# Optimization experiments

Measured on AMD Instinct MI355X. Metric: run time of the kernel, lower is better.

## Reference

```python
import jax, jax.numpy as jnp
import numpy as np

B, S, H, P2 = 64, 512, 768, 46  # batch, seq, hidden, num_p*2


def setup_inputs() -> dict:
    key = jax.random.key(0)
    k1, k2, k3, k4 = jax.random.split(key, 4)
    hidden_states = jax.random.normal(k1, (B, S, H), dtype=jnp.float32)
    # subject start/end indices must lie within the valid (masked-in) prefix
    lengths = jax.random.randint(k2, (B,), S // 4, S + 1)  # cue lengths per sample
    input_mask = (jnp.arange(S)[None, :] < lengths[:, None]).astype(jnp.int32)
    ids = jax.random.randint(k3, (B, 2), 0, S // 4)
    batch_subject_ids = jnp.sort(ids, axis=1).astype(jnp.int32)
    W = jax.random.normal(k4, (P2, H), dtype=jnp.float32) * (1.0 / np.sqrt(H))
    b = jnp.zeros((P2,), dtype=jnp.float32)
    return {"hidden_states": hidden_states, "batch_subject_ids": batch_subject_ids,
            "input_mask": input_mask, "W": W, "b": b}


def reference(hidden_states, batch_subject_ids, input_mask, W, b):
    # per-sample subject embedding: h[b, start] + h[b, end]  -> [B, H]
    batch_idx = jnp.arange(hidden_states.shape[0])
    s = (hidden_states[batch_idx, batch_subject_ids[:, 0]]
         + hidden_states[batch_idx, batch_subject_ids[:, 1]])
    # broadcast-add s to the first cue_len positions of each sample
    cue_len = jnp.sum(input_mask, axis=1)  # [B]
    pos_mask = (jnp.arange(hidden_states.shape[1])[None, :] < cue_len[:, None])  # [B, S]
    h = hidden_states + s[:, None, :] * pos_mask[:, :, None].astype(hidden_states.dtype)
    # linear + sigmoid^4 (dropout is identity in eval mode)
    logits = jnp.einsum('bsh,ph->bsp', h, W) + b
    return jax.nn.sigmoid(logits) ** 4
```

## Files before the change

kernel.cpp:

```cpp
#include <hip/hip_runtime.h>

#define SEQ 512
#define HID 768
#define P2  46
#define BLK 512
#define MT  128
#define KC  32
#define NC  (HID / KC)
#define WST 776

typedef short bf16x8 __attribute__((ext_vector_type(8)));
typedef float f32x4  __attribute__((ext_vector_type(4)));

__device__ __forceinline__ unsigned short f2bf(float f) {
  union { float f; unsigned int u; } v; v.f = f;
  return (unsigned short)((v.u + 0x7FFFu + ((v.u >> 16) & 1u)) >> 16);
}

__device__ __forceinline__ void gl_lds16(const float* g, void* l) {
  __builtin_amdgcn_global_load_lds(
      (const __attribute__((address_space(1))) void*)g,
      (__attribute__((address_space(3))) void*)l, 16, 0, 0);
}

__global__ __launch_bounds__(BLK, 2) void fused_kernel(const float* __restrict__ h,
                                                       const int* __restrict__ ids,
                                                       const int* __restrict__ mask,
                                                       const float* __restrict__ W,
                                                       const float* __restrict__ bias,
                                                       float* __restrict__ out) {
  __shared__ __align__(16) unsigned short wlds[48 * WST];
  __shared__ __align__(16) float hbuf[4][MT * KC];
  __shared__ __align__(16) float s_lds[HID];
  __shared__ float q_lds[48];

  const int tid  = threadIdx.x;
  const int lane = tid & 63, wv = tid >> 6;
  const int mr   = lane & 15, qd = lane >> 4;
  const int row0 = blockIdx.x * MT;
  const int b    = row0 >> 9;

  auto issueChunk = [&](int c) {
    int buf = c & 3;
    #pragma unroll
    for (int j = 0; j < 2; ++j) {
      int sb  = (wv << 7) + (j << 6);
      int s   = sb + lane;
      int row = s >> 3;
      int cc  = (s & 7) ^ (row & 7);
      const float* g = h + (size_t)(row0 + row) * HID + c * KC + (cc << 2);
      gl_lds16(g, (void*)&hbuf[buf][sb << 2]);
    }
  };

  issueChunk(0); issueChunk(1); issueChunk(2);

  for (int i = tid; i < (2 * WST) / 2; i += BLK)
    ((unsigned int*)(wlds + 46 * WST))[i] = 0u;
  for (int i = tid; i < (P2 * HID) / 4; i += BLK) {
    int r  = i / 192;
    int c0 = (i - r * 192) * 4;
    float4 w4 = *(const float4*)(W + (size_t)r * HID + c0);
    ushort4 v;
    v.x = f2bf(w4.x); v.y = f2bf(w4.y); v.z = f2bf(w4.z); v.w = f2bf(w4.w);
    *(ushort4*)&wlds[r * WST + c0] = v;
  }
  {
    int i0 = ids[b * 2 + 0], i1 = ids[b * 2 + 1];
    const float* r0 = h + ((size_t)b * SEQ + i0) * HID;
    const float* r1 = h + ((size_t)b * SEQ + i1) * HID;
    for (int k = tid; k < HID; k += BLK) s_lds[k] = r0[k] + r1[k];
  }
  __syncthreads();

  if (tid < P2 * 4) {
    int p = tid >> 2, kq = tid & 3;
    const float4* wp = (const float4*)(W + (size_t)p * HID + kq * 192);
    float acc = 0.f;
    #pragma unroll 8
    for (int j = 0; j < 48; ++j) {
      float4 w4 = wp[j];
      int k = kq * 192 + j * 4;
      acc += s_lds[k] * w4.x + s_lds[k + 1] * w4.y
           + s_lds[k + 2] * w4.z + s_lds[k + 3] * w4.w;
    }
    acc += __shfl_xor(acc, 1, 64);
    acc += __shfl_xor(acc, 2, 64);
    if (kq == 0) q_lds[p] = acc;
  }
  __syncthreads();

  f32x4 acc[3];
  #pragma unroll
  for (int nt = 0; nt < 3; ++nt) acc[nt] = f32x4{0.f, 0.f, 0.f, 0.f};

  const int rA   = (wv << 4) + mr;
  const int base = (rA & 15) * 8 + (wv << 7);
  const int r7   = mr & 7;

  #pragma unroll
  for (int c = 0; c < NC; ++c) {
    const int fut = NC - 1 - c;
    if (fut >= 2)      asm volatile("s_waitcnt vmcnt(4)" ::: "memory");
    else if (fut == 1) asm volatile("s_waitcnt vmcnt(2)" ::: "memory");
    else               asm volatile("s_waitcnt vmcnt(0)" ::: "memory");

    const float* hb = &hbuf[c & 3][0];
    int cc0 = qd << 1;
    float4 x0 = *(const float4*)&hb[(base + (cc0 ^ r7)) << 2];
    float4 x1 = *(const float4*)&hb[(base + ((cc0 + 1) ^ r7)) << 2];
    bf16x8 a;
    a[0] = (short)f2bf(x0.x); a[1] = (short)f2bf(x0.y);
    a[2] = (short)f2bf(x0.z); a[3] = (short)f2bf(x0.w);
    a[4] = (short)f2bf(x1.x); a[5] = (short)f2bf(x1.y);
    a[6] = (short)f2bf(x1.z); a[7] = (short)f2bf(x1.w);
    #pragma unroll
    for (int nt = 0; nt < 3; ++nt) {
      bf16x8 bb = *(const bf16x8*)&wlds[((nt << 4) + mr) * WST + c * KC + (qd << 3)];
      acc[nt] = __builtin_amdgcn_mfma_f32_16x16x32_bf16(a, bb, acc[nt], 0, 0, 0);
    }
    if (c + 3 < NC) issueChunk(c + 3);
  }

  int mrow[4];
  #pragma unroll
  for (int i = 0; i < 4; ++i)
    mrow[i] = mask[row0 + (wv << 4) + (qd << 2) + i];

  #pragma unroll
  for (int nt = 0; nt < 3; ++nt) {
    int p = (nt << 4) + mr;
    if (p < P2) {
      float bv = bias[p];
      float qv = q_lds[p];
      #pragma unroll
      for (int i = 0; i < 4; ++i) {
        int row = row0 + (wv << 4) + (qd << 2) + i;
        float x = acc[nt][i] + bv + (mrow[i] ? qv : 0.f);
        float sg = 1.f / (1.f + __expf(-x));
        sg *= sg; sg *= sg;
        out[(size_t)row * P2 + p] = sg;
      }
    }
  }
}

extern "C" void kernel_launch(void* const* d_in, const int* in_sizes, int n_in,
                              void* d_out, int out_size, void* d_ws, size_t ws_size,
                              hipStream_t stream) {
  const float* h    = (const float*)d_in[0];
  const int*   ids  = (const int*)d_in[1];
  const int*   mask = (const int*)d_in[2];
  const float* W    = (const float*)d_in[3];
  const float* bias = (const float*)d_in[4];
  float* out = (float*)d_out;

  fused_kernel<<<dim3((64 * SEQ) / MT), BLK, 0, stream>>>(h, ids, mask, W, bias, out);
}
```

Baseline: 169.5 us.

## Split K dimension across two wave groups with LDS reduction in 1024-thread blocks

Doubles the block to 16 waves and splits the hidden dimension in half, so each group of 8 waves computes a partial 128x48 MFMA tile over 12 K-chunks with double buffering. Partial accumulators are then combined through LDS before the sigmoid epilogue. The subject-projection dot product is redistributed so each wave reduces whole rows with shuffles. The goal is more waves in flight to hide global-load latency, at the cost of an extra LDS reduction, shallower prefetch and larger blocks per CU.

Result: faster. 163.4 us (-3.6%).

```diff
diff --git a/kernel.cpp b/kernel.cpp
--- a/kernel.cpp
+++ b/kernel.cpp
@@ -3,10 +3,10 @@
 #define SEQ 512
 #define HID 768
 #define P2  46
-#define BLK 512
+#define BLK 1024
 #define MT  128
 #define KC  32
-#define NC  (HID / KC)
+#define HK  12
 #define WST 776
 
 typedef short bf16x8 __attribute__((ext_vector_type(8)));
@@ -23,92 +23,88 @@
       (__attribute__((address_space(3))) void*)l, 16, 0, 0);
 }
 
-__global__ __launch_bounds__(BLK, 2) void fused_kernel(const float* __restrict__ h,
+__global__ __launch_bounds__(BLK, 4) void fused_kernel(const float* __restrict__ h,
                                                        const int* __restrict__ ids,
                                                        const int* __restrict__ mask,
                                                        const float* __restrict__ W,
                                                        const float* __restrict__ bias,
                                                        float* __restrict__ out) {
   __shared__ __align__(16) unsigned short wlds[48 * WST];
-  __shared__ __align__(16) float hbuf[4][MT * KC];
+  __shared__ __align__(16) float hbuf[2][16 * 128 * 4];
   __shared__ __align__(16) float s_lds[HID];
   __shared__ float q_lds[48];
 
   const int tid  = threadIdx.x;
   const int lane = tid & 63, wv = tid >> 6;
+  const int g    = wv & 7,  kh = wv >> 3;
   const int mr   = lane & 15, qd = lane >> 4;
   const int row0 = blockIdx.x * MT;
   const int b    = row0 >> 9;
+  const int c0   = kh * HK;
 
   auto issueChunk = [&](int c) {
-    int buf = c & 3;
+    int buf = c & 1;
     #pragma unroll
     for (int j = 0; j < 2; ++j) {
-      int sb  = (wv << 7) + (j << 6);
-      int s   = sb + lane;
-      int row = s >> 3;
-      int cc  = (s & 7) ^ (row & 7);
-      const float* g = h + (size_t)(row0 + row) * HID + c * KC + (cc << 2);
-      gl_lds16(g, (void*)&hbuf[buf][sb << 2]);
+      int sw = (j << 6) + lane;
+      int rl = sw >> 3;
+      int cc = (sw & 7) ^ (rl & 7);
+      const float* gp = h + (size_t)(row0 + (g << 4) + rl) * HID + c * KC + (cc << 2);
+      gl_lds16(gp, (void*)&hbuf[buf][((wv << 7) + (j << 6)) << 2]);
     }
   };
 
-  issueChunk(0); issueChunk(1); issueChunk(2);
+  issueChunk(c0); issueChunk(c0 + 1);
 
-  for (int i = tid; i < (2 * WST) / 2; i += BLK)
+  for (int i = tid; i < WST; i += BLK)
     ((unsigned int*)(wlds + 46 * WST))[i] = 0u;
   for (int i = tid; i < (P2 * HID) / 4; i += BLK) {
     int r  = i / 192;
-    int c0 = (i - r * 192) * 4;
-    float4 w4 = *(const float4*)(W + (size_t)r * HID + c0);
+    int cb = (i - r * 192) << 2;
+    float4 w4 = *(const float4*)(W + (size_t)r * HID + cb);
     ushort4 v;
     v.x = f2bf(w4.x); v.y = f2bf(w4.y); v.z = f2bf(w4.z); v.w = f2bf(w4.w);
-    *(ushort4*)&wlds[r * WST + c0] = v;
+    *(ushort4*)&wlds[r * WST + cb] = v;
   }
   {
     int i0 = ids[b * 2 + 0], i1 = ids[b * 2 + 1];
     const float* r0 = h + ((size_t)b * SEQ + i0) * HID;
     const float* r1 = h + ((size_t)b * SEQ + i1) * HID;
-    for (int k = tid; k < HID; k += BLK) s_lds[k] = r0[k] + r1[k];
+    if (tid < HID) s_lds[tid] = r0[tid] + r1[tid];
   }
   __syncthreads();
 
-  if (tid < P2 * 4) {
-    int p = tid >> 2, kq = tid & 3;
-    const float4* wp = (const float4*)(W + (size_t)p * HID + kq * 192);
-    float acc = 0.f;
-    #pragma unroll 8
-    for (int j = 0; j < 48; ++j) {
-      float4 w4 = wp[j];
-      int k = kq * 192 + j * 4;
-      acc += s_lds[k] * w4.x + s_lds[k + 1] * w4.y
-           + s_lds[k + 2] * w4.z + s_lds[k + 3] * w4.w;
+  #pragma unroll
+  for (int t = 0; t < 3; ++t) {
+    int p = wv * 3 + t;
+    if (p < P2) {
+      const float* wp = W + (size_t)p * HID;
+      float acc = 0.f;
+      #pragma unroll
+      for (int j = 0; j < HID / 64; ++j)
+        acc += s_lds[(j << 6) + lane] * wp[(j << 6) + lane];
+      #pragma unroll
+      for (int off = 32; off; off >>= 1)
+        acc += __shfl_down(acc, off, 64);
+      if (lane == 0) q_lds[p] = acc;
     }
-    acc += __shfl_xor(acc, 1, 64);
-    acc += __shfl_xor(acc, 2, 64);
-    if (kq == 0) q_lds[p] = acc;
   }
-  __syncthreads();
 
   f32x4 acc[3];
   #pragma unroll
   for (int nt = 0; nt < 3; ++nt) acc[nt] = f32x4{0.f, 0.f, 0.f, 0.f};
 
-  const int rA   = (wv << 4) + mr;
-  const int base = (rA & 15) * 8 + (wv << 7);
-  const int r7   = mr & 7;
+  const int r7    = mr & 7;
+  const int abase = (wv << 7) + (mr << 3);
 
   #pragma unroll
-  for (int c = 0; c < NC; ++c) {
-    const int fut = NC - 1 - c;
-    if (fut >= 2)      asm volatile("s_waitcnt vmcnt(4)" ::: "memory");
-    else if (fut == 1) asm volatile("s_waitcnt vmcnt(2)" ::: "memory");
-    else               asm volatile("s_waitcnt vmcnt(0)" ::: "memory");
-
-    const float* hb = &hbuf[c & 3][0];
-    int cc0 = qd << 1;
-    float4 x0 = *(const float4*)&hb[(base + (cc0 ^ r7)) << 2];
-    float4 x1 = *(const float4*)&hb[(base + ((cc0 + 1) ^ r7)) << 2];
+  for (int i = 0; i < HK; ++i) {
+    int c = c0 + i;
+    if (i < HK - 1) asm volatile("s_waitcnt vmcnt(2)" ::: "memory");
+    else            asm volatile("s_waitcnt vmcnt(0)" ::: "memory");
+    const float* hb = hbuf[c & 1];
+    float4 x0 = *(const float4*)&hb[(abase + (((qd << 1) + 0) ^ r7)) << 2];
+    float4 x1 = *(const float4*)&hb[(abase + (((qd << 1) + 1) ^ r7)) << 2];
     bf16x8 a;
     a[0] = (short)f2bf(x0.x); a[1] = (short)f2bf(x0.y);
     a[2] = (short)f2bf(x0.z); a[3] = (short)f2bf(x0.w);
@@ -119,27 +115,41 @@
       bf16x8 bb = *(const bf16x8*)&wlds[((nt << 4) + mr) * WST + c * KC + (qd << 3)];
       acc[nt] = __builtin_amdgcn_mfma_f32_16x16x32_bf16(a, bb, acc[nt], 0, 0, 0);
     }
-    if (c + 3 < NC) issueChunk(c + 3);
+    if (i + 2 < HK) issueChunk(c + 2);
   }
 
-  int mrow[4];
-  #pragma unroll
-  for (int i = 0; i < 4; ++i)
-    mrow[i] = mask[row0 + (wv << 4) + (qd << 2) + i];
+  __syncthreads();
+  float* rb = (float*)hbuf;
+  if (kh == 1) {
+    #pragma unroll
+    for (int nt = 0; nt < 3; ++nt)
+      *(f32x4*)&rb[((g << 6) + lane) * 12 + (nt << 2)] = acc[nt];
+  }
+  __syncthreads();
+  if (kh == 0) {
+    #pragma unroll
+    for (int nt = 0; nt < 3; ++nt)
+      acc[nt] += *(const f32x4*)&rb[((g << 6) + lane) * 12 + (nt << 2)];
 
-  #pragma unroll
-  for (int nt = 0; nt < 3; ++nt) {
-    int p = (nt << 4) + mr;
-    if (p < P2) {
-      float bv = bias[p];
-      float qv = q_lds[p];
-      #pragma unroll
-      for (int i = 0; i < 4; ++i) {
-        int row = row0 + (wv << 4) + (qd << 2) + i;
-        float x = acc[nt][i] + bv + (mrow[i] ? qv : 0.f);
-        float sg = 1.f / (1.f + __expf(-x));
-        sg *= sg; sg *= sg;
-        out[(size_t)row * P2 + p] = sg;
+    int mrow[4];
+    #pragma unroll
+    for (int i = 0; i < 4; ++i)
+      mrow[i] = mask[row0 + (g << 4) + (qd << 2) + i];
+
+    #pragma unroll
+    for (int nt = 0; nt < 3; ++nt) {
+      int p = (nt << 4) + mr;
+      if (p < P2) {
+        float bv = bias[p];
+        float qv = q_lds[p];
+        #pragma unroll
+        for (int i = 0; i < 4; ++i) {
+          int row = row0 + (g << 4) + (qd << 2) + i;
+          float x = acc[nt][i] + bv + (mrow[i] ? qv : 0.f);
+          float sg = 1.f / (1.f + __expf(-x));
+          sg *= sg; sg *= sg;
+          out[(size_t)row * P2 + p] = sg;
+        }
       }
     }
   }
```
